# Performance work log

Hardware: AMD Instinct MI355X
Metric: run time of the kernel (lower is better)

The kernel has to match this reference:

```python
import jax, jax.numpy as jnp
import numpy as np

N = 50000        # n_nodes
E = 1_600_000    # n_edges (before self-loops)
D_IN, HID, HEADS, D_OUT = 32, 64, 4, 32
NEG_SLOPE = 0.2  # PyG GATConv default leaky_relu slope


def setup_inputs() -> dict:
    key = jax.random.key(0)
    ks = jax.random.split(key, 10)
    x = jax.random.normal(ks[0], (N, D_IN), jnp.float32)
    edge_index = jax.random.randint(ks[1], (2, E), 0, N, dtype=jnp.int64)
    s = 0.1
    W_gcn = jax.random.normal(ks[2], (D_IN, HID), jnp.float32) * s
    b_gcn = jnp.zeros((HID,), jnp.float32)
    W_gat = jax.random.normal(ks[3], (HID, HEADS * HID), jnp.float32) * s
    att_src = jax.random.normal(ks[4], (HEADS, HID), jnp.float32) * s
    att_dst = jax.random.normal(ks[5], (HEADS, HID), jnp.float32) * s
    b_gat = jnp.zeros((HEADS * HID,), jnp.float32)
    W_fc = jax.random.normal(ks[6], (HEADS * HID, D_OUT), jnp.float32) * s
    b_fc = jnp.zeros((D_OUT,), jnp.float32)
    return dict(x=x, edge_index=edge_index, W_gcn=W_gcn, b_gcn=b_gcn,
                W_gat=W_gat, att_src=att_src, att_dst=att_dst, b_gat=b_gat,
                W_fc=W_fc, b_fc=b_fc)


def _add_self_loops(edge_index, n):
    loop = jnp.arange(n, dtype=edge_index.dtype)
    src = jnp.concatenate([edge_index[0], loop])
    dst = jnp.concatenate([edge_index[1], loop])
    return src, dst


def _gcn(x, src, dst, W, b):
    h = x @ W                                               # (N, HID)
    deg = jax.ops.segment_sum(jnp.ones_like(src, jnp.float32), dst, N)
    dinv = jnp.where(deg > 0, jax.lax.rsqrt(deg), 0.0)
    norm = dinv[src] * dinv[dst]                            # (E+N,)
    out = jax.ops.segment_sum(h[src] * norm[:, None], dst, N)
    return out + b


def _gat(x, src, dst, W, att_src, att_dst, b):
    h = (x @ W).reshape(N, HEADS, HID)                      # (N, H, C)
    a_s = jnp.einsum('nhc,hc->nh', h, att_src)              # (N, H)
    a_d = jnp.einsum('nhc,hc->nh', h, att_dst)
    e = jax.nn.leaky_relu(a_s[src] + a_d[dst], NEG_SLOPE)   # (E+N, H)
    # softmax over incoming edges per destination node
    m = jax.ops.segment_max(e, dst, N)                      # every dst has a self-loop
    w = jnp.exp(e - m[dst])
    denom = jax.ops.segment_sum(w, dst, N)
    alpha = w / denom[dst]                                  # (E+N, H)
    out = jax.ops.segment_sum(h[src] * alpha[:, :, None], dst, N)
    return out.reshape(N, HEADS * HID) + b


def reference(x, edge_index, W_gcn, b_gcn, W_gat, att_src, att_dst, b_gat, W_fc, b_fc):
    src, dst = _add_self_loops(edge_index, N)
    h = jax.nn.relu(_gcn(x, src, dst, W_gcn, b_gcn))        # dropout: eval mode (identity)
    h = jax.nn.relu(_gat(h, src, dst, W_gat, att_src, att_dst, b_gat))
    return h @ W_fc + b_fc
```

## Files before the change

kernel.cpp:

```cpp
#include <hip/hip_runtime.h>
#include <hip/hip_bf16.h>
#include <hip/hip_fp16.h>
#include <math.h>

#define N_NODES 50000
#define N_EDGES 1600000
#define D_IN    32
#define HID     64
#define HEADS   4
#define D_OUT   32
#define NEG_SLOPE 0.2f
#define NTILES 3125

#define CQG 64
#define CQA 32

#define NBKT 196
#define NBLK_A 391
#define TILE_A 4096
#define GH (NBKT * NBLK_A)
#define NSB 300
#define CAP 10240

typedef _Float16 half8 __attribute__((ext_vector_type(8)));
typedef float    f32x4 __attribute__((ext_vector_type(4)));
typedef float    f32x2 __attribute__((ext_vector_type(2)));

__global__ __launch_bounds__(256) void histA(const int* __restrict__ edge,
                                             int* __restrict__ ghist) {
    __shared__ int hist[4][NBKT];
    int t = threadIdx.x, wv = t >> 6;
    for (int i = t; i < 4 * NBKT; i += 256) ((int*)hist)[i] = 0;
    __syncthreads();
    int base = blockIdx.x * TILE_A;
#pragma unroll
    for (int k = 0; k < 16; k++) {
        int i = base + k * 256 + t;
        if (i < N_EDGES) atomicAdd(&hist[wv][edge[N_EDGES + i] >> 8], 1);
    }
    __syncthreads();
    for (int b = t; b < NBKT; b += 256)
        ghist[b * NBLK_A + blockIdx.x] = hist[0][b] + hist[1][b] + hist[2][b] + hist[3][b];
}

__global__ __launch_bounds__(256) void scanB1(const int* __restrict__ g,
                                              int* __restrict__ bsum) {
    int t = threadIdx.x;
    int i = blockIdx.x * 256 + t;
    int v = (i < GH) ? g[i] : 0;
#pragma unroll
    for (int off = 32; off; off >>= 1) v += __shfl_xor(v, off);
    __shared__ int ws[4];
    if ((t & 63) == 0) ws[t >> 6] = v;
    __syncthreads();
    if (t == 0) bsum[blockIdx.x] = ws[0] + ws[1] + ws[2] + ws[3];
}

__global__ __launch_bounds__(320) void scanB2_attvec(int* __restrict__ bsum,
                                                     const float* __restrict__ W,
                                                     const float* __restrict__ att_s,
                                                     const float* __restrict__ att_d,
                                                     float* __restrict__ vsrc,
                                                     float* __restrict__ vdst) {
    int t = threadIdx.x, lane = t & 63, wv = t >> 6;
    if (blockIdx.x == 0) {
        int v = (t < NSB) ? bsum[t] : 0;
        int inc = v;
#pragma unroll
        for (int d = 1; d < 64; d <<= 1) {
            int u = __shfl_up(inc, d);
            if (lane >= d) inc += u;
        }
        __shared__ int ws[5];
        if (lane == 63) ws[wv] = inc;
        __syncthreads();
        int add = 0;
#pragma unroll
        for (int j = 0; j < 5; j++) if (j < wv) add += ws[j];
        if (t < NSB) bsum[t] = add + inc - v;
    } else if (t < 256) {
        int h = t >> 6, k = t & 63;
        float s_ = 0.f, d_ = 0.f;
#pragma unroll 8
        for (int c = 0; c < 64; c++) {
            float w = W[k * 256 + h * 64 + c];
            s_ += w * att_s[h * 64 + c];
            d_ += w * att_d[h * 64 + c];
        }
        vsrc[h * 64 + k] = s_;
        vdst[h * 64 + k] = d_;
    }
}

__global__ __launch_bounds__(256) void scanB3(int* __restrict__ g,
                                              const int* __restrict__ bsum) {
    int t = threadIdx.x, lane = t & 63, wv = t >> 6;
    int i = blockIdx.x * 256 + t;
    int v = (i < GH) ? g[i] : 0;
    int inc = v;
#pragma unroll
    for (int d = 1; d < 64; d <<= 1) {
        int u = __shfl_up(inc, d);
        if (lane >= d) inc += u;
    }
    __shared__ int ws[4];
    if (lane == 63) ws[wv] = inc;
    __syncthreads();
    int add = 0;
#pragma unroll
    for (int j = 0; j < 4; j++) if (j < wv) add += ws[j];
    if (i < GH) g[i] = bsum[blockIdx.x] + add + inc - v;
}

__global__ __launch_bounds__(512) void scatterC(const int* __restrict__ edge,
                                                const int* __restrict__ ghist,
                                                unsigned* __restrict__ tmp) {
    __shared__ int cur[NBKT];
    int t = threadIdx.x;
    if (t < NBKT) cur[t] = ghist[t * NBLK_A + blockIdx.x];
    __syncthreads();
    int base = blockIdx.x * TILE_A;
#pragma unroll
    for (int k = 0; k < 8; k++) {
        int i = base + k * 512 + t;
        if (i < N_EDGES) {
            int s = edge[i], d = edge[N_EDGES + i];
            int pos = atomicAdd(&cur[d >> 8], 1);
            tmp[pos] = ((unsigned)d << 16) | (unsigned)s;
        }
    }
}

__global__ __launch_bounds__(512) void sortD(const unsigned* __restrict__ tmp,
                                             const int* __restrict__ ghist,
                                             unsigned short* __restrict__ colidx,
                                             int* __restrict__ rowptr,
                                             float* __restrict__ dinv) {
    __shared__ unsigned char  dl8[CAP];
    __shared__ unsigned short s16[CAP];
    __shared__ unsigned short o16[CAP];
    __shared__ int hist[8][256];
    __shared__ int excl[256];
    __shared__ int wsum[4];
    int t = threadIdx.x, lane = t & 63, wv = t >> 6;
    int b = blockIdx.x;
    int lo = ghist[b * NBLK_A];
    int hi = (b < NBKT - 1) ? ghist[(b + 1) * NBLK_A] : N_EDGES;
    int size = hi - lo;
    if (size > CAP) size = CAP;
    for (int i = t; i < 8 * 256; i += 512) ((int*)hist)[i] = 0;
    __syncthreads();
    for (int i = t; i < size; i += 512) {
        unsigned key = tmp[lo + i];
        int dl = (key >> 16) & 255;
        dl8[i] = (unsigned char)dl;
        s16[i] = (unsigned short)(key & 0xFFFF);
        atomicAdd(&hist[wv][dl], 1);
    }
    __syncthreads();
    int h = 0, inc = 0;
    if (t < 256) {
        h = hist[0][t] + hist[1][t] + hist[2][t] + hist[3][t]
          + hist[4][t] + hist[5][t] + hist[6][t] + hist[7][t];
        inc = h;
#pragma unroll
        for (int d = 1; d < 64; d <<= 1) {
            int u = __shfl_up(inc, d);
            if (lane >= d) inc += u;
        }
        if (lane == 63) wsum[wv] = inc;
    }
    __syncthreads();
    if (t < 256) {
        int add = 0;
#pragma unroll
        for (int j = 0; j < 4; j++) if (j < wv) add += wsum[j];
        int ex = inc - h + add;
        excl[t] = ex;
        int node = b * 256 + t;
        if (node < N_NODES) {
            rowptr[node] = lo + ex;
            dinv[node]   = rsqrtf((float)(h + 1));
        }
    }
    if (b == NBKT - 1 && t == 0) rowptr[N_NODES] = N_EDGES;
    __syncthreads();
    for (int i = t; i < size; i += 512) {
        int pos = atomicAdd(&excl[dl8[i]], 1);
        o16[pos] = s16[i];
    }
    __syncthreads();
    for (int i = t; i < size; i += 512) colidx[lo + i] = o16[i];
}

__global__ __launch_bounds__(256) void gemm1(const float* __restrict__ x,
                                             const float* __restrict__ W,
                                             const float* __restrict__ dinv,
                                             __half* __restrict__ h,
                                             __half* __restrict__ h1) {
    __shared__ float Wl[D_IN * HID];
    int t = threadIdx.x;
    if (blockIdx.x == 0 && t < HID) {
        h [(size_t)N_NODES * HID + t] = __float2half(0.f);
        h1[(size_t)N_NODES * HID + t] = __float2half(0.f);
    }
    for (int i = t; i < D_IN * HID; i += 256) Wl[i] = W[i];
    __syncthreads();
    int c = t & 63, rw = t >> 6;
    int r0 = blockIdx.x * 32;
#pragma unroll
    for (int rr = 0; rr < 8; rr++) {
        int r = r0 + rr * 4 + rw;
        if (r >= N_NODES) break;
        const float4* xr4 = (const float4*)(x + r * D_IN);
        float acc = 0.f;
#pragma unroll
        for (int k4 = 0; k4 < D_IN / 4; k4++) {
            float4 xv = xr4[k4];
            int k = k4 * 4;
            acc += xv.x * Wl[(k+0)*HID + c] + xv.y * Wl[(k+1)*HID + c]
                 + xv.z * Wl[(k+2)*HID + c] + xv.w * Wl[(k+3)*HID + c];
        }
        h[r * HID + c] = __float2half(acc * dinv[r]);
    }
}

__global__ __launch_bounds__(256) void gcn_agg(const __half* __restrict__ h,
                                               const int* __restrict__ rowptr,
                                               const unsigned short* __restrict__ colidx,
                                               const float* __restrict__ dinv,
                                               const float* __restrict__ b,
                                               const float* __restrict__ vsrc,
                                               const float* __restrict__ vdst,
                                               __half* __restrict__ h1,
                                               float* __restrict__ as_o,
                                               float* __restrict__ ad_o) {
    __shared__ int sbuf[4][8][CQG + 1];
    int lane = threadIdx.x & 63, wv = threadIdx.x >> 6;
    int oct = lane >> 3, ol = lane & 7;
    int n = blockIdx.x * 32 + wv * 8 + oct;
    int nn = min(n, N_NODES - 1);
    int rp = rowptr[nn], re = rowptr[nn + 1];
    int deg = (n < N_NODES) ? (re - rp) : 0;
    int dm = deg;
    dm = max(dm, __shfl_xor(dm, 8));
    dm = max(dm, __shfl_xor(dm, 16));
    dm = max(dm, __shfl_xor(dm, 32));
    f32x4 a0 = {0.f,0.f,0.f,0.f}, a1 = {0.f,0.f,0.f,0.f};
    const __half* hp = h + ol * 8;
    int* sq = sbuf[wv][oct];
    for (int cb = 0; cb < dm; cb += CQG) {
        int m  = min(CQG, max(deg - cb, 0));
        int mm = min(CQG, dm - cb);
        int mm8 = (mm + 7) & ~7;
        for (int j = ol; j < m; j += 8)
            sq[j] = (int)colidx[rp + cb + j] * HID;
        for (int j = m + ol; j < mm8; j += 8)
            sq[j] = N_NODES * HID;
        for (int i0 = 0; i0 < mm8; i0 += 8) {
            float4 raw[8];
#pragma unroll
            for (int k = 0; k < 8; k++)
                raw[k] = *(const float4*)(hp + sq[i0 + k]);
#pragma unroll
            for (int k = 0; k < 8; k++) {
                __half2 g0 = __builtin_bit_cast(__half2, raw[k].x);
                __half2 g1 = __builtin_bit_cast(__half2, raw[k].y);
                __half2 g2 = __builtin_bit_cast(__half2, raw[k].z);
                __half2 g3 = __builtin_bit_cast(__half2, raw[k].w);
                float2 f0 = __half22float2(g0), f1 = __half22float2(g1);
                float2 f2 = __half22float2(g2), f3 = __half22float2(g3);
                a0.x += f0.x; a0.y += f0.y; a0.z += f1.x; a0.w += f1.y;
                a1.x += f2.x; a1.y += f2.y; a1.z += f3.x; a1.w += f3.y;
            }
        }
    }
    {
        float4 raw = *(const float4*)(hp + nn * HID);
        __half2 g0 = __builtin_bit_cast(__half2, raw.x);
        __half2 g1 = __builtin_bit_cast(__half2, raw.y);
        __half2 g2 = __builtin_bit_cast(__half2, raw.z);
        __half2 g3 = __builtin_bit_cast(__half2, raw.w);
        float2 f0 = __half22float2(g0), f1 = __half22float2(g1);
        float2 f2 = __half22float2(g2), f3 = __half22float2(g3);
        a0.x += f0.x; a0.y += f0.y; a0.z += f1.x; a0.w += f1.y;
        a1.x += f2.x; a1.y += f2.y; a1.z += f3.x; a1.w += f3.y;
    }
    float dn = dinv[nn];
    const float4 bb0 = *(const float4*)&b[ol * 8];
    const float4 bb1 = *(const float4*)&b[ol * 8 + 4];
    float v0 = fmaxf(a0.x * dn + bb0.x, 0.f);
    float v1 = fmaxf(a0.y * dn + bb0.y, 0.f);
    float v2 = fmaxf(a0.z * dn + bb0.z, 0.f);
    float v3 = fmaxf(a0.w * dn + bb0.w, 0.f);
    float v4 = fmaxf(a1.x * dn + bb1.x, 0.f);
    float v5 = fmaxf(a1.y * dn + bb1.y, 0.f);
    float v6 = fmaxf(a1.z * dn + bb1.z, 0.f);
    float v7 = fmaxf(a1.w * dn + bb1.w, 0.f);
    if (n < N_NODES) {
        __half2 p0 = __floats2half2_rn(v0, v1);
        __half2 p1 = __floats2half2_rn(v2, v3);
        __half2 p2 = __floats2half2_rn(v4, v5);
        __half2 p3 = __floats2half2_rn(v6, v7);
        float4 pk;
        pk.x = __builtin_bit_cast(float, p0);
        pk.y = __builtin_bit_cast(float, p1);
        pk.z = __builtin_bit_cast(float, p2);
        pk.w = __builtin_bit_cast(float, p3);
        *(float4*)&h1[n * HID + ol * 8] = pk;
    }
#pragma unroll
    for (int hh = 0; hh < 4; hh++) {
        const float4 s0 = *(const float4*)&vsrc[hh * 64 + ol * 8];
        const float4 s1 = *(const float4*)&vsrc[hh * 64 + ol * 8 + 4];
        const float4 d0 = *(const float4*)&vdst[hh * 64 + ol * 8];
        const float4 d1 = *(const float4*)&vdst[hh * 64 + ol * 8 + 4];
        float vs = v0*s0.x + v1*s0.y + v2*s0.z + v3*s0.w
                 + v4*s1.x + v5*s1.y + v6*s1.z + v7*s1.w;
        float vd = v0*d0.x + v1*d0.y + v2*d0.z + v3*d0.w
                 + v4*d1.x + v5*d1.y + v6*d1.z + v7*d1.w;
#pragma unroll
        for (int off = 4; off > 0; off >>= 1) {
            vs += __shfl_xor(vs, off);
            vd += __shfl_xor(vd, off);
        }
        if (ol == 0 && n < N_NODES) {
            as_o[n * 4 + hh] = vs;
            ad_o[n * 4 + hh] = vd;
        }
    }
}

__global__ __launch_bounds__(256) void gat_agg(const __half* __restrict__ h1,
                                               const int* __restrict__ rowptr,
                                               const unsigned short* __restrict__ colidx,
                                               const float* __restrict__ a_s,
                                               const float* __restrict__ a_d,
                                               __half* __restrict__ u) {
    __shared__ float4 wbuf[4][8][CQA + 1];
    __shared__ int    sbuf[4][8][CQA + 1];
    int lane = threadIdx.x & 63, wv = threadIdx.x >> 6;
    int oct = lane >> 3, ol = lane & 7;
    int n = blockIdx.x * 32 + wv * 8 + oct;
    int nn = min(n, N_NODES - 1);
    int rp = rowptr[nn], re = rowptr[nn + 1];
    int deg = (n < N_NODES) ? (re - rp) : 0;
    int dm = deg;
    dm = max(dm, __shfl_xor(dm, 8));
    dm = max(dm, __shfl_xor(dm, 16));
    dm = max(dm, __shfl_xor(dm, 32));
    float4 ad4 = *(const float4*)&a_d[nn * 4];

    float dnx = 0.f, dny = 0.f, dnz = 0.f, dnw = 0.f;
    f32x4 accA[4], accB[4];
#pragma unroll
    for (int hh = 0; hh < 4; hh++) { accA[hh] = (f32x4){0.f,0.f,0.f,0.f}; accB[hh] = (f32x4){0.f,0.f,0.f,0.f}; }
    const __half* hp = h1 + ol * 8;
    int*    sq = sbuf[wv][oct];
    float4* wq = wbuf[wv][oct];
    for (int cb = 0; cb < dm; cb += CQA) {
        int m  = min(CQA, max(deg - cb, 0));
        int mm = min(CQA, dm - cb);
        int mm8 = (mm + 7) & ~7;
        for (int j = ol; j < m; j += 8) {
            int s = colidx[rp + cb + j];
            float4 a = *(const float4*)&a_s[s * 4];
            float vx = a.x + ad4.x; vx = fmaxf(vx, NEG_SLOPE * vx);
            float vy = a.y + ad4.y; vy = fmaxf(vy, NEG_SLOPE * vy);
            float vz = a.z + ad4.z; vz = fmaxf(vz, NEG_SLOPE * vz);
            float vw = a.w + ad4.w; vw = fmaxf(vw, NEG_SLOPE * vw);
            float wx = __expf(vx), wy = __expf(vy);
            float wz = __expf(vz), ww = __expf(vw);
            dnx += wx; dny += wy; dnz += wz; dnw += ww;
            sq[j] = s * HID;
            wq[j] = make_float4(wx, wy, wz, ww);
        }
        for (int j = m + ol; j < mm8; j += 8) {
            sq[j] = N_NODES * HID;
            wq[j] = make_float4(0.f, 0.f, 0.f, 0.f);
        }
        for (int i0 = 0; i0 < mm8; i0 += 8) {
            float4 raw[8];
#pragma unroll
            for (int k = 0; k < 8; k++)
                raw[k] = *(const float4*)(hp + sq[i0 + k]);
#pragma unroll
            for (int k = 0; k < 8; k++) {
                float4 w4 = wq[i0 + k];
                __half2 g0 = __builtin_bit_cast(__half2, raw[k].x);
                __half2 g1 = __builtin_bit_cast(__half2, raw[k].y);
                __half2 g2 = __builtin_bit_cast(__half2, raw[k].z);
                __half2 g3 = __builtin_bit_cast(__half2, raw[k].w);
                float2 f0 = __half22float2(g0), f1 = __half22float2(g1);
                float2 f2 = __half22float2(g2), f3 = __half22float2(g3);
                f32x4 flo = {f0.x, f0.y, f1.x, f1.y};
                f32x4 fhi = {f2.x, f2.y, f3.x, f3.y};
                f32x4 wxv = {w4.x, w4.x, w4.x, w4.x};
                f32x4 wyv = {w4.y, w4.y, w4.y, w4.y};
                f32x4 wzv = {w4.z, w4.z, w4.z, w4.z};
                f32x4 wwv = {w4.w, w4.w, w4.w, w4.w};
                accA[0] += wxv * flo; accB[0] += wxv * fhi;
                accA[1] += wyv * flo; accB[1] += wyv * fhi;
                accA[2] += wzv * flo; accB[2] += wzv * fhi;
                accA[3] += wwv * flo; accB[3] += wwv * fhi;
            }
        }
    }
#pragma unroll
    for (int off = 4; off > 0; off >>= 1) {
        dnx += __shfl_xor(dnx, off);
        dny += __shfl_xor(dny, off);
        dnz += __shfl_xor(dnz, off);
        dnw += __shfl_xor(dnw, off);
    }
    float4 asn = *(const float4*)&a_s[nn * 4];
    float sx = asn.x + ad4.x; sx = fmaxf(sx, NEG_SLOPE * sx);
    float sy = asn.y + ad4.y; sy = fmaxf(sy, NEG_SLOPE * sy);
    float sz = asn.z + ad4.z; sz = fmaxf(sz, NEG_SLOPE * sz);
    float sw = asn.w + ad4.w; sw = fmaxf(sw, NEG_SLOPE * sw);
    float wsx = __expf(sx), wsy = __expf(sy);
    float wsz = __expf(sz), wsw = __expf(sw);
    dnx += wsx; dny += wsy; dnz += wsz; dnw += wsw;
    {
        float4 raw = *(const float4*)(hp + nn * HID);
        __half2 g0 = __builtin_bit_cast(__half2, raw.x);
        __half2 g1 = __builtin_bit_cast(__half2, raw.y);
        __half2 g2 = __builtin_bit_cast(__half2, raw.z);
        __half2 g3 = __builtin_bit_cast(__half2, raw.w);
        float2 f0 = __half22float2(g0), f1 = __half22float2(g1);
        float2 f2 = __half22float2(g2), f3 = __half22float2(g3);
        f32x4 flo = {f0.x, f0.y, f1.x, f1.y};
        f32x4 fhi = {f2.x, f2.y, f3.x, f3.y};
        accA[0] += (f32x4){wsx,wsx,wsx,wsx} * flo; accB[0] += (f32x4){wsx,wsx,wsx,wsx} * fhi;
        accA[1] += (f32x4){wsy,wsy,wsy,wsy} * flo; accB[1] += (f32x4){wsy,wsy,wsy,wsy} * fhi;
        accA[2] += (f32x4){wsz,wsz,wsz,wsz} * flo; accB[2] += (f32x4){wsz,wsz,wsz,wsz} * fhi;
        accA[3] += (f32x4){wsw,wsw,wsw,wsw} * flo; accB[3] += (f32x4){wsw,wsw,wsw,wsw} * fhi;
    }
    if (n < N_NODES) {
        float r4[4] = {1.f / dnx, 1.f / dny, 1.f / dnz, 1.f / dnw};
        __half* up = u + (size_t)n * 256 + ol * 8;
#pragma unroll
        for (int hh = 0; hh < 4; hh++) {
            float r = r4[hh];
            __half2 p0 = __floats2half2_rn(accA[hh].x * r, accA[hh].y * r);
            __half2 p1 = __floats2half2_rn(accA[hh].z * r, accA[hh].w * r);
            __half2 p2 = __floats2half2_rn(accB[hh].x * r, accB[hh].y * r);
            __half2 p3 = __floats2half2_rn(accB[hh].z * r, accB[hh].w * r);
            float4 pk;
            pk.x = __builtin_bit_cast(float, p0);
            pk.y = __builtin_bit_cast(float, p1);
            pk.z = __builtin_bit_cast(float, p2);
            pk.w = __builtin_bit_cast(float, p3);
            *(float4*)&up[hh * 64] = pk;
        }
    }
}

__global__ __launch_bounds__(256) void gemm23(const __half* __restrict__ u,
                                              const float* __restrict__ Wg,
                                              const float* __restrict__ bg,
                                              const float* __restrict__ Wf,
                                              const float* __restrict__ bf,
                                              float* __restrict__ out) {
    __shared__ __half h2s[64][264];
    int lane = threadIdx.x & 63, hd = threadIdx.x >> 6;
    int quad = lane >> 4, l16 = lane & 15;
    half8 Bg[4][2];
#pragma unroll
    for (int nt = 0; nt < 4; nt++)
#pragma unroll
        for (int kc = 0; kc < 2; kc++) {
            const float* wp = Wg + (kc * 32 + quad * 8) * 256 + hd * 64 + nt * 16 + l16;
#pragma unroll
            for (int j = 0; j < 8; j++)
                Bg[nt][kc][j] = (_Float16)wp[j * 256];
        }
    float bbg[4];
#pragma unroll
    for (int nt = 0; nt < 4; nt++) bbg[nt] = bg[hd * 64 + nt * 16 + l16];
    half8 Bf[2][8];
#pragma unroll
    for (int nt = 0; nt < 2; nt++)
#pragma unroll
        for (int kc = 0; kc < 8; kc++) {
            const float* wp = Wf + (kc * 32 + quad * 8) * 32 + nt * 16 + l16;
#pragma unroll
            for (int j = 0; j < 8; j++)
                Bf[nt][kc][j] = (_Float16)wp[j * 32];
        }
    float bb0 = bf[l16], bb1 = bf[16 + l16];

    int t0 = blockIdx.x * 4;
#pragma unroll
    for (int i = 0; i < 4; i++) {
        int rt = t0 + i;
        if (rt >= NTILES) break;
        const __half* up = u + ((size_t)(rt * 16 + l16)) * 256 + hd * 64 + quad * 8;
        half8 A0 = *(const half8*)(const void*)up;
        half8 A1 = *(const half8*)(const void*)(up + 32);
        f32x4 acc[4];
#pragma unroll
        for (int nt = 0; nt < 4; nt++) {
            acc[nt] = (f32x4){0.f, 0.f, 0.f, 0.f};
            acc[nt] = __builtin_amdgcn_mfma_f32_16x16x32_f16(A0, Bg[nt][0], acc[nt], 0, 0, 0);
            acc[nt] = __builtin_amdgcn_mfma_f32_16x16x32_f16(A1, Bg[nt][1], acc[nt], 0, 0, 0);
        }
#pragma unroll
        for (int nt = 0; nt < 4; nt++) {
            int col = hd * 64 + nt * 16 + l16;
#pragma unroll
            for (int reg = 0; reg < 4; reg++)
                h2s[i * 16 + quad * 4 + reg][col] = __float2half(fmaxf(acc[nt][reg] + bbg[nt], 0.f));
        }
    }
    __syncthreads();
    int rt = t0 + hd;
    if (rt < NTILES) {
        f32x4 acc0 = {0.f, 0.f, 0.f, 0.f};
        f32x4 acc1 = {0.f, 0.f, 0.f, 0.f};
#pragma unroll
        for (int kc = 0; kc < 8; kc++) {
            half8 A = *(const half8*)(const void*)&h2s[hd * 16 + l16][kc * 32 + quad * 8];
            acc0 = __builtin_amdgcn_mfma_f32_16x16x32_f16(A, Bf[0][kc], acc0, 0, 0, 0);
            acc1 = __builtin_amdgcn_mfma_f32_16x16x32_f16(A, Bf[1][kc], acc1, 0, 0, 0);
        }
#pragma unroll
        for (int reg = 0; reg < 4; reg++) {
            int row = rt * 16 + quad * 4 + reg;
            out[row * 32 + l16]      = acc0[reg] + bb0;
            out[row * 32 + 16 + l16] = acc1[reg] + bb1;
        }
    }
}

extern "C" void kernel_launch(void* const* d_in, const int* in_sizes, int n_in,
                              void* d_out, int out_size, void* d_ws, size_t ws_size,
                              hipStream_t stream) {
    const float* x      = (const float*)d_in[0];
    const int*   edge   = (const int*)  d_in[1];
    const float* W_gcn  = (const float*)d_in[2];
    const float* b_gcn  = (const float*)d_in[3];
    const float* W_gat  = (const float*)d_in[4];
    const float* att_s  = (const float*)d_in[5];
    const float* att_d  = (const float*)d_in[6];
    const float* b_gat  = (const float*)d_in[7];
    const float* W_fc   = (const float*)d_in[8];
    const float* b_fc   = (const float*)d_in[9];
    float* out = (float*)d_out;

    char* p = (char*)d_ws;
    auto alloc = [&](size_t bytes) {
        char* q = p;
        p += (bytes + 255) & ~(size_t)255;
        return q;
    };
    __half* h     = (__half*)alloc((size_t)(N_NODES + 1) * HID * 2);
    __half* h1    = (__half*)alloc((size_t)(N_NODES + 1) * HID * 2);
    __half* u     = (__half*)alloc((size_t)N_NODES * 256 * 2);
    float* as_a   = (float*)alloc((size_t)N_NODES * 4 * 4);
    float* ad_a   = (float*)alloc((size_t)N_NODES * 4 * 4);
    float* dinv   = (float*)alloc((size_t)N_NODES * 4);
    int*   rowptr = (int*)  alloc((size_t)(N_NODES + 1) * 4);
    unsigned short* colidx = (unsigned short*)alloc((size_t)N_EDGES * 2);
    int*   ghist  = (int*)  alloc((size_t)GH * 4);
    int*   bsum   = (int*)  alloc((size_t)NSB * 4);
    unsigned* tmp = (unsigned*)alloc((size_t)N_EDGES * 4);
    float* vsrc   = (float*)alloc((size_t)HEADS * HID * 4);
    float* vdst   = (float*)alloc((size_t)HEADS * HID * 4);

    histA        <<<NBLK_A, 256, 0, stream>>>(edge, ghist);
    scanB1       <<<NSB, 256, 0, stream>>>(ghist, bsum);
    scanB2_attvec<<<2, 320, 0, stream>>>(bsum, W_gat, att_s, att_d, vsrc, vdst);
    scanB3       <<<NSB, 256, 0, stream>>>(ghist, bsum);
    scatterC     <<<NBLK_A, 512, 0, stream>>>(edge, ghist, tmp);
    sortD        <<<NBKT, 512, 0, stream>>>(tmp, ghist, colidx, rowptr, dinv);

    gemm1   <<<(N_NODES + 31) / 32, 256, 0, stream>>>(x, W_gcn, dinv, h, h1);
    gcn_agg <<<(N_NODES + 31) / 32, 256, 0, stream>>>(h, rowptr, colidx, dinv, b_gcn,
                                                      vsrc, vdst, h1, as_a, ad_a);

    gat_agg <<<(N_NODES + 31) / 32, 256, 0, stream>>>(h1, rowptr, colidx, as_a, ad_a, u);

    gemm23  <<<(NTILES + 3) / 4, 256, 0, stream>>>(u, W_gat, b_gat, W_fc, b_fc, out);
}
```

Measured before the change: 210.2 us.

## Use 128-node buckets and a two-level per-bucket scan to cut kernel launches

Bucket width for the destination counting sort drops from 256 to 128 nodes, so there are 391 buckets and sortD runs 391 blocks with half the LDS each, which gives more parallelism and occupancy. The three-kernel global scan is replaced by a per-bucket scan kernel plus a small scan over bucket totals fused with the attention-vector precompute, removing one launch. scatterC and sortD now add the bucket start offsets separately. The per-bucket capacity is halved to 5120, which risks silent truncation if a bucket holds more edges than that, though the mean is about 4100.

```diff
diff --git a/kernel.cpp b/kernel.cpp
--- a/kernel.cpp
+++ b/kernel.cpp
@@ -15,12 +15,11 @@
 #define CQG 64
 #define CQA 32
 
-#define NBKT 196
+#define NBKT 391
 #define NBLK_A 391
 #define TILE_A 4096
 #define GH (NBKT * NBLK_A)
-#define NSB 300
-#define CAP 10240
+#define CAP 5120
 
 typedef _Float16 half8 __attribute__((ext_vector_type(8)));
 typedef float    f32x4 __attribute__((ext_vector_type(4)));
@@ -36,88 +35,101 @@
 #pragma unroll
     for (int k = 0; k < 16; k++) {
         int i = base + k * 256 + t;
-        if (i < N_EDGES) atomicAdd(&hist[wv][edge[N_EDGES + i] >> 8], 1);
+        if (i < N_EDGES) atomicAdd(&hist[wv][edge[N_EDGES + i] >> 7], 1);
     }
     __syncthreads();
     for (int b = t; b < NBKT; b += 256)
         ghist[b * NBLK_A + blockIdx.x] = hist[0][b] + hist[1][b] + hist[2][b] + hist[3][b];
 }
 
-__global__ __launch_bounds__(256) void scanB1(const int* __restrict__ g,
-                                              int* __restrict__ bsum) {
-    int t = threadIdx.x;
-    int i = blockIdx.x * 256 + t;
-    int v = (i < GH) ? g[i] : 0;
-#pragma unroll
-    for (int off = 32; off; off >>= 1) v += __shfl_xor(v, off);
-    __shared__ int ws[4];
-    if ((t & 63) == 0) ws[t >> 6] = v;
-    __syncthreads();
-    if (t == 0) bsum[blockIdx.x] = ws[0] + ws[1] + ws[2] + ws[3];
-}
-
-__global__ __launch_bounds__(320) void scanB2_attvec(int* __restrict__ bsum,
-                                                     const float* __restrict__ W,
-                                                     const float* __restrict__ att_s,
-                                                     const float* __restrict__ att_d,
-                                                     float* __restrict__ vsrc,
-                                                     float* __restrict__ vdst) {
+__global__ __launch_bounds__(256) void scanBkt(int* __restrict__ g,
+                                               int* __restrict__ btot) {
+    __shared__ int vv[512];
+    __shared__ int wsum[4];
+    int t = threadIdx.x, lane = t & 63, wv = t >> 6;
+    int b = blockIdx.x;
+    int* gb = g + b * NBLK_A;
+    vv[t]       = (t       < NBLK_A) ? gb[t]       : 0;
+    vv[t + 256] = (t + 256 < NBLK_A) ? gb[t + 256] : 0;
+    __syncthreads();
+    int v0 = vv[2 * t], v1 = vv[2 * t + 1];
+    int s = v0 + v1;
+    int inc = s;
+#pragma unroll
+    for (int d = 1; d < 64; d <<= 1) {
+        int u_ = __shfl_up(inc, d);
+        if (lane >= d) inc += u_;
+    }
+    if (lane == 63) wsum[wv] = inc;
+    __syncthreads();
+    int add = 0;
+#pragma unroll
+    for (int j = 0; j < 4; j++) if (j < wv) add += wsum[j];
+    int ex = add + inc - s;
+    __syncthreads();
+    vv[2 * t]     = ex;
+    vv[2 * t + 1] = ex + v0;
+    __syncthreads();
+    if (t       < NBLK_A) gb[t]       = vv[t];
+    if (t + 256 < NBLK_A) gb[t + 256] = vv[t + 256];
+    if (t == 255) btot[b] = add + inc;
+}
+
+__global__ __launch_bounds__(256) void scanTot_attvec(const int* __restrict__ btot,
+                                                      int* __restrict__ bstart,
+                                                      const float* __restrict__ W,
+                                                      const float* __restrict__ att_s,
+                                                      const float* __restrict__ att_d,
+                                                      float* __restrict__ vsrc,
+                                                      float* __restrict__ vdst) {
     int t = threadIdx.x, lane = t & 63, wv = t >> 6;
     if (blockIdx.x == 0) {
-        int v = (t < NSB) ? bsum[t] : 0;
-        int inc = v;
+        __shared__ int vv[512];
+        __shared__ int wsum[4];
+        vv[t]       = (t       < NBKT) ? btot[t]       : 0;
+        vv[t + 256] = (t + 256 < NBKT) ? btot[t + 256] : 0;
+        __syncthreads();
+        int v0 = vv[2 * t], v1 = vv[2 * t + 1];
+        int s = v0 + v1;
+        int inc = s;
 #pragma unroll
         for (int d = 1; d < 64; d <<= 1) {
-            int u = __shfl_up(inc, d);
-            if (lane >= d) inc += u;
-        }
-        __shared__ int ws[5];
-        if (lane == 63) ws[wv] = inc;
+            int u_ = __shfl_up(inc, d);
+            if (lane >= d) inc += u_;
+        }
+        if (lane == 63) wsum[wv] = inc;
         __syncthreads();
         int add = 0;
 #pragma unroll
-        for (int j = 0; j < 5; j++) if (j < wv) add += ws[j];
-        if (t < NSB) bsum[t] = add + inc - v;
-    } else if (t < 256) {
-        int h = t >> 6, k = t & 63;
+        for (int j = 0; j < 4; j++) if (j < wv) add += wsum[j];
+        int ex = add + inc - s;
+        __syncthreads();
+        vv[2 * t]     = ex;
+        vv[2 * t + 1] = ex + v0;
+        __syncthreads();
+        if (t       < NBKT) bstart[t]       = vv[t];
+        if (t + 256 < NBKT) bstart[t + 256] = vv[t + 256];
+    } else {
+        int hh = t >> 6, k = t & 63;
         float s_ = 0.f, d_ = 0.f;
 #pragma unroll 8
         for (int c = 0; c < 64; c++) {
-            float w = W[k * 256 + h * 64 + c];
-            s_ += w * att_s[h * 64 + c];
-            d_ += w * att_d[h * 64 + c];
-        }
-        vsrc[h * 64 + k] = s_;
-        vdst[h * 64 + k] = d_;
-    }
-}
-
-__global__ __launch_bounds__(256) void scanB3(int* __restrict__ g,
-                                              const int* __restrict__ bsum) {
-    int t = threadIdx.x, lane = t & 63, wv = t >> 6;
-    int i = blockIdx.x * 256 + t;
-    int v = (i < GH) ? g[i] : 0;
-    int inc = v;
-#pragma unroll
-    for (int d = 1; d < 64; d <<= 1) {
-        int u = __shfl_up(inc, d);
-        if (lane >= d) inc += u;
-    }
-    __shared__ int ws[4];
-    if (lane == 63) ws[wv] = inc;
-    __syncthreads();
-    int add = 0;
-#pragma unroll
-    for (int j = 0; j < 4; j++) if (j < wv) add += ws[j];
-    if (i < GH) g[i] = bsum[blockIdx.x] + add + inc - v;
+            float w = W[k * 256 + hh * 64 + c];
+            s_ += w * att_s[hh * 64 + c];
+            d_ += w * att_d[hh * 64 + c];
+        }
+        vsrc[hh * 64 + k] = s_;
+        vdst[hh * 64 + k] = d_;
+    }
 }
 
 __global__ __launch_bounds__(512) void scatterC(const int* __restrict__ edge,
                                                 const int* __restrict__ ghist,
+                                                const int* __restrict__ bstart,
                                                 unsigned* __restrict__ tmp) {
     __shared__ int cur[NBKT];
     int t = threadIdx.x;
-    if (t < NBKT) cur[t] = ghist[t * NBLK_A + blockIdx.x];
+    if (t < NBKT) cur[t] = bstart[t] + ghist[t * NBLK_A + blockIdx.x];
     __syncthreads();
     int base = blockIdx.x * TILE_A;
 #pragma unroll
@@ -125,59 +137,57 @@
         int i = base + k * 512 + t;
         if (i < N_EDGES) {
             int s = edge[i], d = edge[N_EDGES + i];
-            int pos = atomicAdd(&cur[d >> 8], 1);
+            int pos = atomicAdd(&cur[d >> 7], 1);
             tmp[pos] = ((unsigned)d << 16) | (unsigned)s;
         }
     }
 }
 
 __global__ __launch_bounds__(512) void sortD(const unsigned* __restrict__ tmp,
-                                             const int* __restrict__ ghist,
+                                             const int* __restrict__ bstart,
                                              unsigned short* __restrict__ colidx,
                                              int* __restrict__ rowptr,
                                              float* __restrict__ dinv) {
     __shared__ unsigned char  dl8[CAP];
     __shared__ unsigned short s16[CAP];
     __shared__ unsigned short o16[CAP];
-    __shared__ int hist[8][256];
-    __shared__ int excl[256];
-    __shared__ int wsum[4];
+    __shared__ int hist[8][128];
+    __shared__ int excl[128];
+    __shared__ int wsum[2];
     int t = threadIdx.x, lane = t & 63, wv = t >> 6;
     int b = blockIdx.x;
-    int lo = ghist[b * NBLK_A];
-    int hi = (b < NBKT - 1) ? ghist[(b + 1) * NBLK_A] : N_EDGES;
+    int lo = bstart[b];
+    int hi = (b < NBKT - 1) ? bstart[b + 1] : N_EDGES;
     int size = hi - lo;
     if (size > CAP) size = CAP;
-    for (int i = t; i < 8 * 256; i += 512) ((int*)hist)[i] = 0;
+    for (int i = t; i < 8 * 128; i += 512) ((int*)hist)[i] = 0;
     __syncthreads();
     for (int i = t; i < size; i += 512) {
         unsigned key = tmp[lo + i];
-        int dl = (key >> 16) & 255;
+        int dl = (key >> 16) & 127;
         dl8[i] = (unsigned char)dl;
         s16[i] = (unsigned short)(key & 0xFFFF);
         atomicAdd(&hist[wv][dl], 1);
     }
     __syncthreads();
     int h = 0, inc = 0;
-    if (t < 256) {
+    if (t < 128) {
         h = hist[0][t] + hist[1][t] + hist[2][t] + hist[3][t]
           + hist[4][t] + hist[5][t] + hist[6][t] + hist[7][t];
         inc = h;
 #pragma unroll
         for (int d = 1; d < 64; d <<= 1) {
-            int u = __shfl_up(inc, d);
-            if (lane >= d) inc += u;
+            int u_ = __shfl_up(inc, d);
+            if (lane >= d) inc += u_;
         }
         if (lane == 63) wsum[wv] = inc;
     }
     __syncthreads();
-    if (t < 256) {
-        int add = 0;
-#pragma unroll
-        for (int j = 0; j < 4; j++) if (j < wv) add += wsum[j];
+    if (t < 128) {
+        int add = (wv == 1) ? wsum[0] : 0;
         int ex = inc - h + add;
         excl[t] = ex;
-        int node = b * 256 + t;
+        int node = b * 128 + t;
         if (node < N_NODES) {
             rowptr[node] = lo + ex;
             dinv[node]   = rsqrtf((float)(h + 1));
@@ -563,17 +573,17 @@
     int*   rowptr = (int*)  alloc((size_t)(N_NODES + 1) * 4);
     unsigned short* colidx = (unsigned short*)alloc((size_t)N_EDGES * 2);
     int*   ghist  = (int*)  alloc((size_t)GH * 4);
-    int*   bsum   = (int*)  alloc((size_t)NSB * 4);
+    int*   btot   = (int*)  alloc((size_t)NBKT * 4);
+    int*   bstart = (int*)  alloc((size_t)NBKT * 4);
     unsigned* tmp = (unsigned*)alloc((size_t)N_EDGES * 4);
     float* vsrc   = (float*)alloc((size_t)HEADS * HID * 4);
     float* vdst   = (float*)alloc((size_t)HEADS * HID * 4);
 
     histA        <<<NBLK_A, 256, 0, stream>>>(edge, ghist);
-    scanB1       <<<NSB, 256, 0, stream>>>(ghist, bsum);
-    scanB2_attvec<<<2, 320, 0, stream>>>(bsum, W_gat, att_s, att_d, vsrc, vdst);
-    scanB3       <<<NSB, 256, 0, stream>>>(ghist, bsum);
-    scatterC     <<<NBLK_A, 512, 0, stream>>>(edge, ghist, tmp);
-    sortD        <<<NBKT, 512, 0, stream>>>(tmp, ghist, colidx, rowptr, dinv);
+    scanBkt      <<<NBKT, 256, 0, stream>>>(ghist, btot);
+    scanTot_attvec<<<2, 256, 0, stream>>>(btot, bstart, W_gat, att_s, att_d, vsrc, vdst);
+    scatterC     <<<NBLK_A, 512, 0, stream>>>(edge, ghist, bstart, tmp);
+    sortD        <<<NBKT, 512, 0, stream>>>(tmp, bstart, colidx, rowptr, dinv);
 
     gemm1   <<<(N_NODES + 31) / 32, 256, 0, stream>>>(x, W_gcn, dinv, h, h1);
     gcn_agg <<<(N_NODES + 31) / 32, 256, 0, stream>>>(h, rowptr, colidx, dinv, b_gcn,
```

Result: no change. 211.5 us (+0.6%).
